# Performance work log

Hardware: AMD Instinct MI355X
Metric: run time of the kernel (lower is better)

The kernel has to match this reference:

```python
import jax, jax.numpy as jnp
import numpy as np

D_MODEL = 1024
NUM_HEADS = 16
D_HEAD = D_MODEL // NUM_HEADS
LN_EPS = 1e-5


def setup_inputs() -> dict:
    key = jax.random.key(0)
    ks = jax.random.split(key, 10)
    s = 1.0 / np.sqrt(D_MODEL)
    inp = {
        "batch": jax.random.normal(ks[0], (4, 2048, D_MODEL), dtype=jnp.float32),
        "wq": jax.random.uniform(ks[1], (D_MODEL, D_MODEL), jnp.float32, -s, s),
        "bq": jax.random.uniform(ks[2], (D_MODEL,), jnp.float32, -s, s),
        "wk": jax.random.uniform(ks[3], (D_MODEL, D_MODEL), jnp.float32, -s, s),
        "bk": jax.random.uniform(ks[4], (D_MODEL,), jnp.float32, -s, s),
        "wv": jax.random.uniform(ks[5], (D_MODEL, D_MODEL), jnp.float32, -s, s),
        "bv": jax.random.uniform(ks[6], (D_MODEL,), jnp.float32, -s, s),
        "wo": jax.random.uniform(ks[7], (D_MODEL, D_MODEL), jnp.float32, -s, s),
        "bo": jax.random.uniform(ks[8], (D_MODEL,), jnp.float32, -s, s),
        "ln_g": jnp.ones((D_MODEL,), jnp.float32),
        "ln_b": jnp.zeros((D_MODEL,), jnp.float32),
    }
    return inp


def reference(batch, wq, bq, wk, bk, wv, bv, wo, bo, ln_g, ln_b):
    B, S, D = batch.shape
    # QKV projections (torch Linear: x @ W.T + b)
    q = (batch @ wq.T + bq).reshape(B, S, NUM_HEADS, D_HEAD)
    k = (batch @ wk.T + bk).reshape(B, S, NUM_HEADS, D_HEAD)
    v = (batch @ wv.T + bv).reshape(B, S, NUM_HEADS, D_HEAD)
    # attention scores [B, H, S, S]
    scores = jnp.einsum("bqhd,bkhd->bhqk", q, k) / np.sqrt(D_HEAD).astype(np.float32)
    # (original masked_fill is not in-place -> mask has no effect; omitted)
    probs = jax.nn.softmax(scores, axis=-1)
    attn = jnp.einsum("bhqk,bkhd->bqhd", probs, v).reshape(B, S, D)
    residual = attn @ wo.T + bo  # dropout = identity (eval mode)
    x = batch + residual
    mu = jnp.mean(x, axis=-1, keepdims=True)
    var = jnp.mean(jnp.square(x - mu), axis=-1, keepdims=True)
    return (x - mu) / jnp.sqrt(var + LN_EPS) * ln_g + ln_b
```

## Files before the change

### kernel.cpp

```cpp
#include <hip/hip_runtime.h>

typedef __bf16 bf16_t;
typedef __bf16 v8bf __attribute__((ext_vector_type(8)));
typedef __bf16 v4bf __attribute__((ext_vector_type(4)));
typedef float  v4f  __attribute__((ext_vector_type(4)));

#define D_MODEL 1024
#define NHEAD   16
#define DHEAD   64
#define SEQ     2048
#define BATCH   4
#define ROWS    (BATCH*SEQ)

#define GLD16(g, l) __builtin_amdgcn_global_load_lds( \
    (const __attribute__((address_space(1))) void*)(g), \
    (__attribute__((address_space(3))) void*)(l), 16, 0, 0)

__global__ __launch_bounds__(256) void k_prep(const float* __restrict__ batch,
                                              const float* __restrict__ wq,
                                              const float* __restrict__ wk,
                                              const float* __restrict__ wv,
                                              const float* __restrict__ wo,
                                              const float* __restrict__ bq,
                                              const float* __restrict__ bk,
                                              const float* __restrict__ bv,
                                              bf16_t* __restrict__ Xb,
                                              bf16_t* __restrict__ Wqkv,
                                              bf16_t* __restrict__ Wob,
                                              float* __restrict__ bqkv) {
    int bid = blockIdx.x, t = threadIdx.x;
    const float* src; bf16_t* dst; int idx;
    if (bid < 8192)       { src = batch; dst = Xb;             idx = bid * 256 + t; }
    else if (bid < 9216)  { src = wq;    dst = Wqkv;           idx = (bid - 8192) * 256 + t; }
    else if (bid < 10240) { src = wk;    dst = Wqkv + 1048576; idx = (bid - 9216) * 256 + t; }
    else if (bid < 11264) { src = wv;    dst = Wqkv + 2097152; idx = (bid - 10240) * 256 + t; }
    else if (bid < 12288) { src = wo;    dst = Wob;            idx = (bid - 11264) * 256 + t; }
    else {
        int i = (bid - 12288) * 256 + t;
        if (i < 1024) bqkv[i] = bq[i];
        else if (i < 2048) bqkv[i] = bk[i - 1024];
        else if (i < 3072) bqkv[i] = bv[i - 2048];
        return;
    }
    float4 f = ((const float4*)src)[idx];
    v4bf o;
    o[0] = (bf16_t)f.x; o[1] = (bf16_t)f.y; o[2] = (bf16_t)f.z; o[3] = (bf16_t)f.w;
    ((v4bf*)dst)[idx] = o;
}

__global__ __launch_bounds__(256, 3) void k_gemm_bt(
    const bf16_t* __restrict__ A, const bf16_t* __restrict__ Bm,
    const float* __restrict__ bias, const float* __restrict__ resid,
    bf16_t* __restrict__ Cb, float* __restrict__ Cf,
    int M, int N, int K, int qcols, float qmul)
{
    __shared__ bf16_t As[2][128 * 32];
    __shared__ bf16_t Bs[2][128 * 32];

    int nTile = N >> 7;
    int x = blockIdx.x & 7, g = blockIdx.x >> 3;
    int n_idx = g % nTile;
    int m_idx = (g / nTile) * 8 + x;
    int m0 = m_idx << 7;
    int n0 = n_idx << 7;
    int t = threadIdx.x;
    int w = t >> 6, lane = t & 63, quad = lane >> 4, ln = lane & 15;
    int wm = (w >> 1) << 6, wn = (w & 1) << 6;

    int srow = lane >> 2;
    int scol = ((lane & 3) ^ ((lane >> 3) & 3)) << 3;
    const bf16_t* Ag0 = A  + (size_t)(m0 + w * 16 +      srow) * K + scol;
    const bf16_t* Ag1 = A  + (size_t)(m0 + w * 16 + 64 + srow) * K + scol;
    const bf16_t* Bg0 = Bm + (size_t)(n0 + w * 16 +      srow) * K + scol;
    const bf16_t* Bg1 = Bm + (size_t)(n0 + w * 16 + 64 + srow) * K + scol;
    int lo0 = (w * 16) * 32, lo1 = (w * 16 + 64) * 32;

    v4f acc[4][4];
#pragma unroll
    for (int i = 0; i < 4; i++)
#pragma unroll
        for (int j = 0; j < 4; j++) acc[i][j] = (v4f){0.f, 0.f, 0.f, 0.f};

    GLD16(Ag0, &As[0][lo0]);
    GLD16(Ag1, &As[0][lo1]);
    GLD16(Bg0, &Bs[0][lo0]);
    GLD16(Bg1, &Bs[0][lo1]);

    int sw = (ln >> 1) & 3;
    int buf = 0;
    for (int k0 = 0; k0 < K; k0 += 32, buf ^= 1) {
        __syncthreads();
        if (k0 + 32 < K) {
            GLD16(Ag0 + k0 + 32, &As[buf ^ 1][lo0]);
            GLD16(Ag1 + k0 + 32, &As[buf ^ 1][lo1]);
            GLD16(Bg0 + k0 + 32, &Bs[buf ^ 1][lo0]);
            GLD16(Bg1 + k0 + 32, &Bs[buf ^ 1][lo1]);
        }
        v8bf af[4], bfr[4];
#pragma unroll
        for (int mt = 0; mt < 4; mt++)
            af[mt] = *(const v8bf*)&As[buf][(wm + mt * 16 + ln) * 32 + ((quad ^ sw) << 3)];
#pragma unroll
        for (int nt = 0; nt < 4; nt++)
            bfr[nt] = *(const v8bf*)&Bs[buf][(wn + nt * 16 + ln) * 32 + ((quad ^ sw) << 3)];
#pragma unroll
        for (int mt = 0; mt < 4; mt++)
#pragma unroll
            for (int nt = 0; nt < 4; nt++)
                acc[mt][nt] = __builtin_amdgcn_mfma_f32_16x16x32_bf16(af[mt], bfr[nt], acc[mt][nt], 0, 0, 0);
    }

#pragma unroll
    for (int mt = 0; mt < 4; mt++) {
#pragma unroll
        for (int r = 0; r < 4; r++) {
            int row = m0 + wm + mt * 16 + quad * 4 + r;
#pragma unroll
            for (int nt = 0; nt < 4; nt++) {
                int col = n0 + wn + nt * 16 + ln;
                float v = acc[mt][nt][r] + bias[col];
                if (Cf) Cf[(size_t)row * N + col] = v + resid[(size_t)row * N + col];
                else {
                    if (col < qcols) v *= qmul;
                    Cb[(size_t)row * N + col] = (bf16_t)v;
                }
            }
        }
    }
}

__global__ __launch_bounds__(256) void k_transpose_v(const bf16_t* __restrict__ qkv,
                                                     bf16_t* __restrict__ vt) {
    __shared__ bf16_t tile[64 * 72];
    int bid = blockIdx.x;
    int st = bid & 31, bh = bid >> 5, b = bh >> 4, h = bh & 15;
    int t = threadIdx.x;
    const bf16_t* src = qkv + (size_t)(b * SEQ + st * 64) * 3072 + 2048 + h * 64;
#pragma unroll
    for (int i = 0; i < 2; i++) {
        int c = t + i * 256, row = c >> 3, c8 = (c & 7) << 3;
        *(uint4*)&tile[row * 72 + c8] = *(const uint4*)(src + (size_t)row * 3072 + c8);
    }
    __syncthreads();
    bf16_t* dst = vt + (size_t)bh * DHEAD * SEQ + st * 64;
#pragma unroll
    for (int i = 0; i < 2; i++) {
        int c = t + i * 256, d = c >> 3, s8 = (c & 7) << 3;
        v8bf o;
#pragma unroll
        for (int j = 0; j < 8; j++) o[j] = tile[(s8 + j) * 72 + d];
        *(v8bf*)(dst + (size_t)d * SEQ + s8) = o;
    }
}

__global__ __launch_bounds__(256, 2) void k_attn(const bf16_t* __restrict__ qkv,
                                                 const bf16_t* __restrict__ vt,
                                                 bf16_t* __restrict__ attn) {
    __shared__ bf16_t Ks[2][64 * 64];
    __shared__ bf16_t Vs[2][64 * 64];

    int bid = blockIdx.x;
    int xcd = bid & 7, g = bid >> 3;
    int qt = g & 15;
    int bh = ((g >> 4) << 3) | xcd;
    int b = bh >> 4, h = bh & 15;
    int t = threadIdx.x, w = t >> 6, lane = t & 63, quad = lane >> 4, ln = lane & 15;
    int q0 = qt * 128 + w * 32;

    v8bf qf[2][2];
#pragma unroll
    for (int qs = 0; qs < 2; qs++) {
        const bf16_t* Qp = qkv + (size_t)(b * SEQ + q0 + qs * 16 + ln) * 3072 + h * 64 + quad * 8;
        qf[qs][0] = *(const v8bf*)Qp;
        qf[qs][1] = *(const v8bf*)(Qp + 32);
    }

    int srow = lane >> 3;
    int scol = ((lane & 7) ^ ((lane >> 3) & 3) ^ ((w & 1) << 2)) << 3;
    const bf16_t* Kg0 = qkv + (size_t)(b * SEQ + w * 8 +      srow) * 3072 + 1024 + h * 64 + scol;
    const bf16_t* Kg1 = qkv + (size_t)(b * SEQ + w * 8 + 32 + srow) * 3072 + 1024 + h * 64 + scol;
    const bf16_t* Vg0 = vt + (size_t)bh * DHEAD * SEQ + (size_t)(w * 8 +      srow) * SEQ + scol;
    const bf16_t* Vg1 = vt + (size_t)bh * DHEAD * SEQ + (size_t)(w * 8 + 32 + srow) * SEQ + scol;
    int ko0 = (w * 8) * 64, ko1 = (w * 8 + 32) * 64;

    int gk = (ln & 3) | (((ln >> 2) & 1) << 2);
    int gv = (ln & 3) | (((ln >> 3) & 1) << 2);
    int rrbase = ((ln >> 2) << 3) + (ln & 3);
    int o0 = (rrbase) * 64,       o1 = (rrbase + 4) * 64;
    int o2 = (rrbase + 32) * 64,  o3 = (rrbase + 36) * 64;

    const v4f z4 = (v4f){0.f, 0.f, 0.f, 0.f};
    v8bf ones8;
#pragma unroll
    for (int j = 0; j < 8; j++) ones8[j] = (bf16_t)1.0f;

    v4f o[2][4];
#pragma unroll
    for (int qs = 0; qs < 2; qs++)
#pragma unroll
        for (int d = 0; d < 4; d++) o[qs][d] = z4;
    v4f den[2] = {z4, z4};

    GLD16(Kg0, &Ks[0][ko0]);
    GLD16(Kg1, &Ks[0][ko1]);
    GLD16(Vg0, &Vs[0][ko0]);
    GLD16(Vg1, &Vs[0][ko1]);

    int buf = 0;
    for (int kt = 0; kt < SEQ; kt += 64, buf ^= 1) {
        __syncthreads();
        if (kt + 64 < SEQ) {
            GLD16(Kg0 + (size_t)(kt + 64) * 3072, &Ks[buf ^ 1][ko0]);
            GLD16(Kg1 + (size_t)(kt + 64) * 3072, &Ks[buf ^ 1][ko1]);
            GLD16(Vg0 + kt + 64, &Vs[buf ^ 1][ko0]);
            GLD16(Vg1 + kt + 64, &Vs[buf ^ 1][ko1]);
        }

        const bf16_t* Kb = &Ks[buf][0];
        v4f s0[4], s1[4];
        int rof[4] = {o0, o1, o2, o3};
#pragma unroll
        for (int nt = 0; nt < 4; nt++) {
            v8bf kf0 = *(const v8bf*)&Kb[rof[nt] + ((quad ^ gk) << 3)];
            v8bf kf1 = *(const v8bf*)&Kb[rof[nt] + (((quad | 4) ^ gk) << 3)];
            s0[nt] = __builtin_amdgcn_mfma_f32_16x16x32_bf16(kf0, qf[0][0], z4, 0, 0, 0);
            s0[nt] = __builtin_amdgcn_mfma_f32_16x16x32_bf16(kf1, qf[0][1], s0[nt], 0, 0, 0);
            s1[nt] = __builtin_amdgcn_mfma_f32_16x16x32_bf16(kf0, qf[1][0], z4, 0, 0, 0);
            s1[nt] = __builtin_amdgcn_mfma_f32_16x16x32_bf16(kf1, qf[1][1], s1[nt], 0, 0, 0);
        }

#pragma unroll
        for (int tk = 0; tk < 2; tk++) {
            v8bf vfd[4];
#pragma unroll
            for (int d = 0; d < 4; d++)
                vfd[d] = *(const v8bf*)&Vs[buf][(d * 16 + ln) * 64 + (((tk * 4 + quad) ^ gv) << 3)];
#pragma unroll
            for (int qs = 0; qs < 2; qs++) {
                v4f* s = qs ? s1 : s0;
                float e0 = __builtin_amdgcn_exp2f(s[2 * tk][0]);
                float e1 = __builtin_amdgcn_exp2f(s[2 * tk][1]);
                float e2 = __builtin_amdgcn_exp2f(s[2 * tk][2]);
                float e3 = __builtin_amdgcn_exp2f(s[2 * tk][3]);
                float e4 = __builtin_amdgcn_exp2f(s[2 * tk + 1][0]);
                float e5 = __builtin_amdgcn_exp2f(s[2 * tk + 1][1]);
                float e6 = __builtin_amdgcn_exp2f(s[2 * tk + 1][2]);
                float e7 = __builtin_amdgcn_exp2f(s[2 * tk + 1][3]);
                v8bf pf;
                pf[0] = (bf16_t)e0; pf[1] = (bf16_t)e1; pf[2] = (bf16_t)e2; pf[3] = (bf16_t)e3;
                pf[4] = (bf16_t)e4; pf[5] = (bf16_t)e5; pf[6] = (bf16_t)e6; pf[7] = (bf16_t)e7;
                den[qs] = __builtin_amdgcn_mfma_f32_16x16x32_bf16(pf, ones8, den[qs], 0, 0, 0);
#pragma unroll
                for (int d = 0; d < 4; d++)
                    o[qs][d] = __builtin_amdgcn_mfma_f32_16x16x32_bf16(pf, vfd[d], o[qs][d], 0, 0, 0);
            }
        }
    }

#pragma unroll
    for (int qs = 0; qs < 2; qs++) {
        int rowg = b * SEQ + q0 + qs * 16;
#pragma unroll
        for (int r = 0; r < 4; r++) {
            float inv = 1.f / den[qs][r];
#pragma unroll
            for (int d = 0; d < 4; d++)
                attn[(size_t)(rowg + quad * 4 + r) * D_MODEL + h * 64 + d * 16 + ln] =
                    (bf16_t)(o[qs][d][r] * inv);
        }
    }
}

__global__ __launch_bounds__(256) void k_layernorm(const float* __restrict__ y,
                                                   const float* __restrict__ g,
                                                   const float* __restrict__ beta,
                                                   float* __restrict__ out) {
    __shared__ float rs[4], rq[4];
    int row = blockIdx.x, t = threadIdx.x;
    int w = t >> 6, lane = t & 63;
    float4 v = ((const float4*)(y + (size_t)row * D_MODEL))[t];
    float s = v.x + v.y + v.z + v.w;
    float q = v.x * v.x + v.y * v.y + v.z * v.z + v.w * v.w;
#pragma unroll
    for (int off = 1; off < 64; off <<= 1) {
        s += __shfl_xor(s, off);
        q += __shfl_xor(q, off);
    }
    if (lane == 0) { rs[w] = s; rq[w] = q; }
    __syncthreads();
    s = rs[0] + rs[1] + rs[2] + rs[3];
    q = rq[0] + rq[1] + rq[2] + rq[3];
    float mu = s * (1.f / D_MODEL);
    float var = q * (1.f / D_MODEL) - mu * mu;
    float rstd = rsqrtf(var + 1e-5f);
    float4 gg = ((const float4*)g)[t];
    float4 bb = ((const float4*)beta)[t];
    float4 o;
    o.x = (v.x - mu) * rstd * gg.x + bb.x;
    o.y = (v.y - mu) * rstd * gg.y + bb.y;
    o.z = (v.z - mu) * rstd * gg.z + bb.z;
    o.w = (v.w - mu) * rstd * gg.w + bb.w;
    ((float4*)(out + (size_t)row * D_MODEL))[t] = o;
}

extern "C" void kernel_launch(void* const* d_in, const int* in_sizes, int n_in,
                              void* d_out, int out_size, void* d_ws, size_t ws_size,
                              hipStream_t stream) {
    const float* batch = (const float*)d_in[0];
    const float* wq = (const float*)d_in[1];
    const float* bq = (const float*)d_in[2];
    const float* wk = (const float*)d_in[3];
    const float* bk = (const float*)d_in[4];
    const float* wv = (const float*)d_in[5];
    const float* bv = (const float*)d_in[6];
    const float* wo = (const float*)d_in[7];
    const float* bo = (const float*)d_in[8];
    const float* ln_g = (const float*)d_in[9];
    const float* ln_b = (const float*)d_in[10];
    float* out = (float*)d_out;

    char* ws = (char*)d_ws;
    size_t offXb   = 0;
    size_t offWqkv = offXb + (size_t)ROWS * D_MODEL * 2;
    size_t offWo   = offWqkv + (size_t)3072 * 1024 * 2;
    size_t offBias = offWo + (size_t)1024 * 1024 * 2;
    size_t offQKV  = offBias + 3072 * 4;
    size_t offAttn = offQKV + (size_t)ROWS * 3072 * 2;
    size_t total   = offAttn + (size_t)ROWS * D_MODEL * 2;
    if (ws_size < total) return;

    bf16_t* Xb   = (bf16_t*)(ws + offXb);
    bf16_t* Vt   = (bf16_t*)(ws + offXb);
    bf16_t* Wqkv = (bf16_t*)(ws + offWqkv);
    bf16_t* Wob  = (bf16_t*)(ws + offWo);
    float*  bqkv = (float*)(ws + offBias);
    bf16_t* qkv  = (bf16_t*)(ws + offQKV);
    float*  y    = (float*)(ws + offQKV);
    bf16_t* attn = (bf16_t*)(ws + offAttn);

    const float SC = 0.125f * 1.44269504088896f;

    k_prep<<<12300, 256, 0, stream>>>(batch, wq, wk, wv, wo, bq, bk, bv,
                                      Xb, Wqkv, Wob, bqkv);
    k_gemm_bt<<<64 * 24, 256, 0, stream>>>(Xb, Wqkv, bqkv, nullptr, qkv, nullptr,
                                           8192, 3072, 1024, 1024, SC);
    k_transpose_v<<<2048, 256, 0, stream>>>(qkv, Vt);
    k_attn<<<1024, 256, 0, stream>>>(qkv, Vt, attn);
    k_gemm_bt<<<64 * 8, 256, 0, stream>>>(attn, Wob, bo, batch, nullptr, y,
                                          8192, 1024, 1024, 0, 1.0f);
    k_layernorm<<<8192, 256, 0, stream>>>(y, ln_g, ln_b, out);
}
```

Before: 301.6 us.

## Triple-buffer GEMM LDS tiles with partial vmcnt waits

Moves the bf16 GEMM k-loop from double to triple buffering of A/B tiles in LDS. Loads run two k-steps ahead, and each step waits only for the older batch of global-to-LDS loads (vmcnt(4)) instead of draining everything at the barrier. The aim is to hide more global-memory latency behind the MFMA work. LDS use rises from 32 KB to 48 KB per block, which may lower occupancy under launch_bounds(256,3). Correctness now depends on the hand-written waitcnt and barrier ordering.

```diff
diff --git a/kernel.cpp b/kernel.cpp
--- a/kernel.cpp
+++ b/kernel.cpp
@@ -54,8 +54,8 @@
     bf16_t* __restrict__ Cb, float* __restrict__ Cf,
     int M, int N, int K, int qcols, float qmul)
 {
-    __shared__ bf16_t As[2][128 * 32];
-    __shared__ bf16_t Bs[2][128 * 32];
+    __shared__ bf16_t As[3][128 * 32];
+    __shared__ bf16_t Bs[3][128 * 32];
 
     int nTile = N >> 7;
     int x = blockIdx.x & 7, g = blockIdx.x >> 3;
@@ -81,33 +81,44 @@
 #pragma unroll
         for (int j = 0; j < 4; j++) acc[i][j] = (v4f){0.f, 0.f, 0.f, 0.f};
 
-    GLD16(Ag0, &As[0][lo0]);
-    GLD16(Ag1, &As[0][lo1]);
-    GLD16(Bg0, &Bs[0][lo0]);
-    GLD16(Bg1, &Bs[0][lo1]);
+    bf16_t* aPrev = As[2]; bf16_t* aCur = As[0]; bf16_t* aNext = As[1];
+    bf16_t* bPrev = Bs[2]; bf16_t* bCur = Bs[0]; bf16_t* bNext = Bs[1];
+
+    GLD16(Ag0, aCur + lo0);
+    GLD16(Ag1, aCur + lo1);
+    GLD16(Bg0, bCur + lo0);
+    GLD16(Bg1, bCur + lo1);
+    GLD16(Ag0 + 32, aNext + lo0);
+    GLD16(Ag1 + 32, aNext + lo1);
+    GLD16(Bg0 + 32, bNext + lo0);
+    GLD16(Bg1 + 32, bNext + lo1);
 
     int sw = (ln >> 1) & 3;
-    int buf = 0;
-    for (int k0 = 0; k0 < K; k0 += 32, buf ^= 1) {
-        __syncthreads();
-        if (k0 + 32 < K) {
-            GLD16(Ag0 + k0 + 32, &As[buf ^ 1][lo0]);
-            GLD16(Ag1 + k0 + 32, &As[buf ^ 1][lo1]);
-            GLD16(Bg0 + k0 + 32, &Bs[buf ^ 1][lo0]);
-            GLD16(Bg1 + k0 + 32, &Bs[buf ^ 1][lo1]);
+    for (int k0 = 0; k0 < K; k0 += 32) {
+        if (k0 + 32 < K) asm volatile("s_waitcnt vmcnt(4)" ::: "memory");
+        else             asm volatile("s_waitcnt vmcnt(0)" ::: "memory");
+        __builtin_amdgcn_s_barrier();
+        __builtin_amdgcn_sched_barrier(0);
+        if (k0 + 64 < K) {
+            GLD16(Ag0 + k0 + 64, aPrev + lo0);
+            GLD16(Ag1 + k0 + 64, aPrev + lo1);
+            GLD16(Bg0 + k0 + 64, bPrev + lo0);
+            GLD16(Bg1 + k0 + 64, bPrev + lo1);
         }
         v8bf af[4], bfr[4];
 #pragma unroll
         for (int mt = 0; mt < 4; mt++)
-            af[mt] = *(const v8bf*)&As[buf][(wm + mt * 16 + ln) * 32 + ((quad ^ sw) << 3)];
+            af[mt] = *(const v8bf*)&aCur[(wm + mt * 16 + ln) * 32 + ((quad ^ sw) << 3)];
 #pragma unroll
         for (int nt = 0; nt < 4; nt++)
-            bfr[nt] = *(const v8bf*)&Bs[buf][(wn + nt * 16 + ln) * 32 + ((quad ^ sw) << 3)];
+            bfr[nt] = *(const v8bf*)&bCur[(wn + nt * 16 + ln) * 32 + ((quad ^ sw) << 3)];
 #pragma unroll
         for (int mt = 0; mt < 4; mt++)
 #pragma unroll
             for (int nt = 0; nt < 4; nt++)
                 acc[mt][nt] = __builtin_amdgcn_mfma_f32_16x16x32_bf16(af[mt], bfr[nt], acc[mt][nt], 0, 0, 0);
+        bf16_t* ta = aPrev; aPrev = aCur; aCur = aNext; aNext = ta;
+        bf16_t* tb = bPrev; bPrev = bCur; bCur = bNext; bNext = tb;
     }
 
 #pragma unroll
```

After: 298.4 us. Within noise of the previous version (-1.0%).
